# Performance work log

Hardware: AMD Instinct MI355X
Metric: run time of the kernel (lower is better)

Reference implementation:

```python
import jax, jax.numpy as jnp
import numpy as np

R = 8192   # rows of the input matrix (attention sequence dim)
F = 4096   # total input feature columns
L = 2048   # number of gathered columns (len(in_keys))


def setup_inputs() -> dict:
    key = jax.random.key(0)
    k1, k2, k3 = jax.random.split(key, 3)
    inputs = jax.random.normal(k1, (R, F), dtype=jnp.float32)
    in_idxs = jax.random.randint(k2, (L,), 0, F)
    weights = jax.random.normal(k3, (L, 3), dtype=jnp.float32)
    return {"inputs": inputs, "in_idxs": in_idxs, "weights": weights}


def reference(inputs, in_idxs, weights):
    # gather: torch.index_select(inputs, 1, in_idxs) -> [R, L]
    sel = jnp.take(inputs, in_idxs, axis=1)
    # QKV projection: [R, L] @ [L, 3] -> [R, 3]; chunk -> q, k, v each [R, 1]
    qkv = sel @ weights
    q, k, v = qkv[:, 0:1], qkv[:, 1:2], qkv[:, 2:3]
    d_k = q.shape[-1]  # = 1
    # scaled dot-product attention over the row dim: logits [R, R]
    logits = (q @ k.T) / jnp.sqrt(jnp.float32(d_k))
    attn = jax.nn.softmax(logits, axis=-1)
    values = attn @ v  # [R, 1]
    # out = activation(values[-1:, ]) -> [1, 1]
    return jax.nn.sigmoid(values[-1:, :])
```

## Files before the change

### kernel.cpp

```cpp
#include <hip/hip_runtime.h>
#include <math.h>

#define RR 8192
#define FF 4096
#define LL 2048
#define RPB 8

__global__ void zero_wsum(float* __restrict__ w) {
    int i = blockIdx.x * 256 + threadIdx.x;
    if (i < 3 * FF) w[i] = 0.0f;
}

__global__ void scatter_wsum(const int* __restrict__ idx, const float* __restrict__ wts,
                             float* __restrict__ w0, float* __restrict__ w1, float* __restrict__ w2) {
    int l = blockIdx.x * 256 + threadIdx.x;
    if (l < LL) {
        int c = idx[l];
        atomicAdd(w0 + c, wts[l * 3 + 0]);
        atomicAdd(w1 + c, wts[l * 3 + 1]);
        atomicAdd(w2 + c, wts[l * 3 + 2]);
    }
}

__global__ __launch_bounds__(256) void gemv3(const float* __restrict__ in,
                                             const float* __restrict__ w0,
                                             const float* __restrict__ w1,
                                             const float* __restrict__ w2,
                                             float* __restrict__ qarr,
                                             float* __restrict__ karr,
                                             float* __restrict__ varr) {
    const int t  = threadIdx.x;
    const int r0 = blockIdx.x * RPB;

    float acc[RPB][3];
#pragma unroll
    for (int r = 0; r < RPB; ++r) { acc[r][0] = 0.f; acc[r][1] = 0.f; acc[r][2] = 0.f; }

#pragma unroll
    for (int i = 0; i < FF; i += 1024) {
        const int c = i + t * 4;
        const float4 a0 = *(const float4*)(w0 + c);
        const float4 a1 = *(const float4*)(w1 + c);
        const float4 a2 = *(const float4*)(w2 + c);
#pragma unroll
        for (int r = 0; r < RPB; ++r) {
            const float4 x = *(const float4*)(in + (size_t)(r0 + r) * FF + c);
            acc[r][0] += x.x * a0.x + x.y * a0.y + x.z * a0.z + x.w * a0.w;
            acc[r][1] += x.x * a1.x + x.y * a1.y + x.z * a1.z + x.w * a1.w;
            acc[r][2] += x.x * a2.x + x.y * a2.y + x.z * a2.z + x.w * a2.w;
        }
    }

    const int lane = t & 63, wv = t >> 6;
#pragma unroll
    for (int r = 0; r < RPB; ++r)
#pragma unroll
        for (int j = 0; j < 3; ++j)
            for (int o = 32; o > 0; o >>= 1)
                acc[r][j] += __shfl_down(acc[r][j], o);

    __shared__ float sred[4][RPB * 3];
    if (lane == 0) {
#pragma unroll
        for (int r = 0; r < RPB; ++r)
#pragma unroll
            for (int j = 0; j < 3; ++j)
                sred[wv][r * 3 + j] = acc[r][j];
    }
    __syncthreads();
    if (t < RPB * 3) {
        const float s = sred[0][t] + sred[1][t] + sred[2][t] + sred[3][t];
        const int r = t / 3, j = t - r * 3;
        float* dst = (j == 0) ? qarr : (j == 1) ? karr : varr;
        dst[r0 + r] = s;
    }
}

__global__ __launch_bounds__(1024) void finalize(const float* __restrict__ qarr,
                                                 const float* __restrict__ karr,
                                                 const float* __restrict__ varr,
                                                 float* __restrict__ out) {
    const int t = threadIdx.x;
    const float q = qarr[RR - 1];

    float lk[RR / 1024], lv[RR / 1024];
    float m = -INFINITY;
#pragma unroll
    for (int i = 0; i < RR / 1024; ++i) {
        const int r = t + i * 1024;
        lk[i] = q * karr[r];
        lv[i] = varr[r];
        m = fmaxf(m, lk[i]);
    }

    __shared__ float red[16];
    __shared__ float bcast[3];

    for (int o = 32; o > 0; o >>= 1) m = fmaxf(m, __shfl_down(m, o));
    if ((t & 63) == 0) red[t >> 6] = m;
    __syncthreads();
    if (t == 0) {
        float x = red[0];
        for (int i = 1; i < 16; ++i) x = fmaxf(x, red[i]);
        bcast[0] = x;
    }
    __syncthreads();
    m = bcast[0];

    float se = 0.f, sv = 0.f;
#pragma unroll
    for (int i = 0; i < RR / 1024; ++i) {
        const float e = expf(lk[i] - m);
        se += e;
        sv += e * lv[i];
    }
    for (int o = 32; o > 0; o >>= 1) { se += __shfl_down(se, o); sv += __shfl_down(sv, o); }
    __shared__ float red2[16];
    if ((t & 63) == 0) { red[t >> 6] = se; red2[t >> 6] = sv; }
    __syncthreads();
    if (t == 0) {
        float a = 0.f, b = 0.f;
        for (int i = 0; i < 16; ++i) { a += red[i]; b += red2[i]; }
        const float val = b / a;
        out[0] = 1.0f / (1.0f + expf(-val));
    }
}

extern "C" void kernel_launch(void* const* d_in, const int* in_sizes, int n_in,
                              void* d_out, int out_size, void* d_ws, size_t ws_size,
                              hipStream_t stream) {
    const float* inputs = (const float*)d_in[0];
    const int*   idx    = (const int*)d_in[1];
    const float* wts    = (const float*)d_in[2];
    float* out = (float*)d_out;

    float* w0   = (float*)d_ws;
    float* w1   = w0 + FF;
    float* w2   = w1 + FF;
    float* qarr = w2 + FF;
    float* karr = qarr + RR;
    float* varr = karr + RR;

    zero_wsum<<<(3 * FF + 255) / 256, 256, 0, stream>>>(w0);
    scatter_wsum<<<(LL + 255) / 256, 256, 0, stream>>>(idx, wts, w0, w1, w2);
    gemv3<<<RR / RPB, 256, 0, stream>>>(inputs, w0, w1, w2, qarr, karr, varr);
    finalize<<<1, 1024, 0, stream>>>(qarr, karr, varr, out);
}
```

Baseline: 37.87 us.

## Fuse weight scatter, GEMV and partial softmax into one kernel with split reduction

```diff
diff --git a/kernel.cpp b/kernel.cpp
--- a/kernel.cpp
+++ b/kernel.cpp
@@ -5,123 +5,130 @@
 #define FF 4096
 #define LL 2048
 #define RPB 8
+#define TPB 256
+#define NBLK (RR / RPB)
 
-__global__ void zero_wsum(float* __restrict__ w) {
-    int i = blockIdx.x * 256 + threadIdx.x;
-    if (i < 3 * FF) w[i] = 0.0f;
-}
+__global__ __launch_bounds__(TPB) void fused_main(const float* __restrict__ in,
+                                                  const int* __restrict__ idx,
+                                                  const float* __restrict__ wts,
+                                                  float* __restrict__ partials ) {
+    __shared__ float w1s[FF];
+    __shared__ float w2s[FF];
+    __shared__ float redbuf[4][RPB * 2];
+    __shared__ float qred[4];
+    __shared__ float kvrow[RPB * 2];
 
-__global__ void scatter_wsum(const int* __restrict__ idx, const float* __restrict__ wts,
-                             float* __restrict__ w0, float* __restrict__ w1, float* __restrict__ w2) {
-    int l = blockIdx.x * 256 + threadIdx.x;
-    if (l < LL) {
-        int c = idx[l];
-        atomicAdd(w0 + c, wts[l * 3 + 0]);
-        atomicAdd(w1 + c, wts[l * 3 + 1]);
-        atomicAdd(w2 + c, wts[l * 3 + 2]);
+    const int t = threadIdx.x, lane = t & 63, wv = t >> 6;
+    const int r0 = blockIdx.x * RPB;
+
+    for (int i = t; i < FF; i += TPB) { w1s[i] = 0.f; w2s[i] = 0.f; }
+    __syncthreads();
+
+    const float* lastrow = in + (size_t)(RR - 1) * FF;
+    float qp = 0.f;
+#pragma unroll
+    for (int l = t; l < LL; l += TPB) {
+        const int c = idx[l];
+        const float x0 = wts[3 * l + 0];
+        const float x1 = wts[3 * l + 1];
+        const float x2 = wts[3 * l + 2];
+        qp += lastrow[c] * x0;
+        atomicAdd(&w1s[c], x1);
+        atomicAdd(&w2s[c], x2);
+    }
+    for (int o = 32; o > 0; o >>= 1) qp += __shfl_down(qp, o);
+    if (lane == 0) qred[wv] = qp;
+    __syncthreads();
+    const float q = qred[0] + qred[1] + qred[2] + qred[3];
+
+    float acc[RPB][2];
+#pragma unroll
+    for (int r = 0; r < RPB; ++r) { acc[r][0] = 0.f; acc[r][1] = 0.f; }
+
+#pragma unroll
+    for (int i = 0; i < FF; i += TPB * 4) {
+        const int c = i + t * 4;
+        const float4 a1 = *(const float4*)&w1s[c];
+        const float4 a2 = *(const float4*)&w2s[c];
+#pragma unroll
+        for (int r = 0; r < RPB; ++r) {
+            const float4 x = *(const float4*)(in + (size_t)(r0 + r) * FF + c);
+            acc[r][0] += x.x * a1.x + x.y * a1.y + x.z * a1.z + x.w * a1.w;
+            acc[r][1] += x.x * a2.x + x.y * a2.y + x.z * a2.z + x.w * a2.w;
+        }
+    }
+
+#pragma unroll
+    for (int r = 0; r < RPB; ++r)
+#pragma unroll
+        for (int j = 0; j < 2; ++j)
+            for (int o = 32; o > 0; o >>= 1)
+                acc[r][j] += __shfl_down(acc[r][j], o);
+
+    if (lane == 0) {
+#pragma unroll
+        for (int r = 0; r < RPB; ++r) {
+            redbuf[wv][r * 2 + 0] = acc[r][0];
+            redbuf[wv][r * 2 + 1] = acc[r][1];
+        }
+    }
+    __syncthreads();
+    if (t < RPB * 2) kvrow[t] = redbuf[0][t] + redbuf[1][t] + redbuf[2][t] + redbuf[3][t];
+    __syncthreads();
+
+    if (t == 0) {
+        float m = -INFINITY;
+#pragma unroll
+        for (int r = 0; r < RPB; ++r) m = fmaxf(m, q * kvrow[r * 2 + 0]);
+        float se = 0.f, sv = 0.f;
+#pragma unroll
+        for (int r = 0; r < RPB; ++r) {
+            const float e = expf(q * kvrow[r * 2 + 0] - m);
+            se += e;
+            sv += e * kvrow[r * 2 + 1];
+        }
+        partials[blockIdx.x * 3 + 0] = m;
+        partials[blockIdx.x * 3 + 1] = se;
+        partials[blockIdx.x * 3 + 2] = sv;
     }
 }
 
-__global__ __launch_bounds__(256) void gemv3(const float* __restrict__ in,
-                                             const float* __restrict__ w0,
-                                             const float* __restrict__ w1,
-                                             const float* __restrict__ w2,
-                                             float* __restrict__ qarr,
-                                             float* __restrict__ karr,
-                                             float* __restrict__ varr) {
-    const int t  = threadIdx.x;
-    const int r0 = blockIdx.x * RPB;
-
-    float acc[RPB][3];
+__global__ __launch_bounds__(TPB) void combine(const float* __restrict__ partials,
+                                               float* __restrict__ out) {
+    const int t = threadIdx.x, lane = t & 63, wv = t >> 6;
+    float lm[NBLK / TPB], lse[NBLK / TPB], lsv[NBLK / TPB];
+    float m = -INFINITY;
 #pragma unroll
-    for (int r = 0; r < RPB; ++r) { acc[r][0] = 0.f; acc[r][1] = 0.f; acc[r][2] = 0.f; }
-
-#pragma unroll
-    for (int i = 0; i < FF; i += 1024) {
-        const int c = i + t * 4;
-        const float4 a0 = *(const float4*)(w0 + c);
-        const float4 a1 = *(const float4*)(w1 + c);
-        const float4 a2 = *(const float4*)(w2 + c);
-#pragma unroll
-        for (int r = 0; r < RPB; ++r) {
-            const float4 x = *(const float4*)(in + (size_t)(r0 + r) * FF + c);
-            acc[r][0] += x.x * a0.x + x.y * a0.y + x.z * a0.z + x.w * a0.w;
-            acc[r][1] += x.x * a1.x + x.y * a1.y + x.z * a1.z + x.w * a1.w;
-            acc[r][2] += x.x * a2.x + x.y * a2.y + x.z * a2.z + x.w * a2.w;
-        }
+    for (int i = 0; i < NBLK / TPB; ++i) {
+        const int b = t + i * TPB;
+        lm[i]  = partials[b * 3 + 0];
+        lse[i] = partials[b * 3 + 1];
+        lsv[i] = partials[b * 3 + 2];
+        m = fmaxf(m, lm[i]);
     }
 
-    const int lane = t & 63, wv = t >> 6;
-#pragma unroll
-    for (int r = 0; r < RPB; ++r)
-#pragma unroll
-        for (int j = 0; j < 3; ++j)
-            for (int o = 32; o > 0; o >>= 1)
-                acc[r][j] += __shfl_down(acc[r][j], o);
-
-    __shared__ float sred[4][RPB * 3];
-    if (lane == 0) {
-#pragma unroll
-        for (int r = 0; r < RPB; ++r)
-#pragma unroll
-            for (int j = 0; j < 3; ++j)
-                sred[wv][r * 3 + j] = acc[r][j];
-    }
+    __shared__ float red[4], red2[4], red3[4], bcast[1];
+    for (int o = 32; o > 0; o >>= 1) m = fmaxf(m, __shfl_down(m, o));
+    if (lane == 0) red[wv] = m;
     __syncthreads();
-    if (t < RPB * 3) {
-        const float s = sred[0][t] + sred[1][t] + sred[2][t] + sred[3][t];
-        const int r = t / 3, j = t - r * 3;
-        float* dst = (j == 0) ? qarr : (j == 1) ? karr : varr;
-        dst[r0 + r] = s;
-    }
-}
-
-__global__ __launch_bounds__(1024) void finalize(const float* __restrict__ qarr,
-                                                 const float* __restrict__ karr,
-                                                 const float* __restrict__ varr,
-                                                 float* __restrict__ out) {
-    const int t = threadIdx.x;
-    const float q = qarr[RR - 1];
-
-    float lk[RR / 1024], lv[RR / 1024];
-    float m = -INFINITY;
-#pragma unroll
-    for (int i = 0; i < RR / 1024; ++i) {
-        const int r = t + i * 1024;
-        lk[i] = q * karr[r];
-        lv[i] = varr[r];
-        m = fmaxf(m, lk[i]);
-    }
-
-    __shared__ float red[16];
-    __shared__ float bcast[3];
-
-    for (int o = 32; o > 0; o >>= 1) m = fmaxf(m, __shfl_down(m, o));
-    if ((t & 63) == 0) red[t >> 6] = m;
+    if (t == 0) bcast[0] = fmaxf(fmaxf(red[0], red[1]), fmaxf(red[2], red[3]));
     __syncthreads();
-    if (t == 0) {
-        float x = red[0];
-        for (int i = 1; i < 16; ++i) x = fmaxf(x, red[i]);
-        bcast[0] = x;
-    }
-    __syncthreads();
-    m = bcast[0];
+    const float gm = bcast[0];
 
     float se = 0.f, sv = 0.f;
 #pragma unroll
-    for (int i = 0; i < RR / 1024; ++i) {
-        const float e = expf(lk[i] - m);
-        se += e;
-        sv += e * lv[i];
+    for (int i = 0; i < NBLK / TPB; ++i) {
+        const float s = expf(lm[i] - gm);
+        se += lse[i] * s;
+        sv += lsv[i] * s;
     }
     for (int o = 32; o > 0; o >>= 1) { se += __shfl_down(se, o); sv += __shfl_down(sv, o); }
-    __shared__ float red2[16];
-    if ((t & 63) == 0) { red[t >> 6] = se; red2[t >> 6] = sv; }
+    if (lane == 0) { red2[wv] = se; red3[wv] = sv; }
     __syncthreads();
     if (t == 0) {
-        float a = 0.f, b = 0.f;
-        for (int i = 0; i < 16; ++i) { a += red[i]; b += red2[i]; }
-        const float val = b / a;
+        const float S = red2[0] + red2[1] + red2[2] + red2[3];
+        const float V = red3[0] + red3[1] + red3[2] + red3[3];
+        const float val = V / S;
         out[0] = 1.0f / (1.0f + expf(-val));
     }
 }
@@ -132,17 +139,9 @@
     const float* inputs = (const float*)d_in[0];
     const int*   idx    = (const int*)d_in[1];
     const float* wts    = (const float*)d_in[2];
-    float* out = (float*)d_out;
+    float* out      = (float*)d_out;
+    float* partials = (float*)d_ws;
 
-    float* w0   = (float*)d_ws;
-    float* w1   = w0 + FF;
-    float* w2   = w1 + FF;
-    float* qarr = w2 + FF;
-    float* karr = qarr + RR;
-    float* varr = karr + RR;
-
-    zero_wsum<<<(3 * FF + 255) / 256, 256, 0, stream>>>(w0);
-    scatter_wsum<<<(LL + 255) / 256, 256, 0, stream>>>(idx, wts, w0, w1, w2);
-    gemv3<<<RR / RPB, 256, 0, stream>>>(inputs, w0, w1, w2, qarr, karr, varr);
-    finalize<<<1, 1024, 0, stream>>>(qarr, karr, varr, out);
+    fused_main<<<NBLK, TPB, 0, stream>>>(inputs, idx, wts, partials);
+    combine<<<1, TPB, 0, stream>>>(partials, out);
 }
```

Measured after the change: 43.32 us. +14.4%, slower.
